# Performance work log

Measured on AMD Instinct MI355X. Metric: run time of the kernel, lower is better.

## Reference

```python
import jax, jax.numpy as jnp
import numpy as np

D_MODEL = 1024
N_HEADS = 16
HEAD_DIM = D_MODEL // N_HEADS
WINDOW = 256


def setup_inputs() -> dict:
    key = jax.random.key(0)
    k1, k2, k3 = jax.random.split(key, 3)
    x = jax.random.normal(k1, (1, 4096, D_MODEL), dtype=jnp.float32)
    # torch nn.Linear weights: [out_features, in_features]
    W_qkv = jax.random.normal(k2, (3 * D_MODEL, D_MODEL), dtype=jnp.float32) * (D_MODEL ** -0.5)
    W_proj = jax.random.normal(k3, (D_MODEL, D_MODEL), dtype=jnp.float32) * (D_MODEL ** -0.5)
    return {"x": x, "W_qkv": W_qkv, "W_proj": W_proj}


def reference(x, W_qkv, W_proj):
    B, T, D = x.shape
    H, Hd = N_HEADS, HEAD_DIM
    qkv = (x @ W_qkv.T).reshape(B, T, 3, H, Hd)
    qkv = jnp.transpose(qkv, (2, 0, 3, 1, 4))  # [3, B, H, T, Hd]
    q, k, v = qkv[0], qkv[1], qkv[2]
    # causal + sliding-window mask: allowed iff 0 <= i - j < WINDOW
    i = jnp.arange(T)[:, None]
    j = jnp.arange(T)[None, :]
    mask = (j <= i) & (j >= i - (WINDOW - 1))  # [T, T] bool
    scale = Hd ** -0.5
    attn = jnp.einsum('bhid,bhjd->bhij', q, k) * scale
    attn = jnp.where(mask, attn, -jnp.inf)
    attn = jax.nn.softmax(attn, axis=-1)
    out = jnp.einsum('bhij,bhjd->bhid', attn, v)  # [B, H, T, Hd]
    out = jnp.transpose(out, (0, 2, 1, 3)).reshape(B, T, D)
    return out @ W_proj.T
```

## Files before the change

### kernel.cpp

```cpp
#include <hip/hip_runtime.h>
#include <hip/hip_bf16.h>


#define T_SEQ   4096
#define DM      1024
#define NH      16
#define HD      64
#define WIN     256

typedef unsigned short u16_t;
typedef u16_t  u16v8 __attribute__((ext_vector_type(8)));
typedef __bf16 bf16v8 __attribute__((ext_vector_type(8)));
typedef float  f32v4 __attribute__((ext_vector_type(4)));

__device__ __forceinline__ f32v4 mfma_bf16(u16v8 a, u16v8 b, f32v4 c) {
    return __builtin_amdgcn_mfma_f32_16x16x32_bf16(
        __builtin_bit_cast(bf16v8, a), __builtin_bit_cast(bf16v8, b), c, 0, 0, 0);
}

__device__ __forceinline__ u16_t f2bf(float f) {
    unsigned u = __builtin_bit_cast(unsigned, f);
    u += 0x7fffu + ((u >> 16) & 1u);
    return (u16_t)(u >> 16);
}

__device__ __forceinline__ float exp2_fast(float x) {
    return __builtin_amdgcn_exp2f(x);
}

__device__ __forceinline__ void gload_lds16(const u16_t* g, u16_t* l) {
    __builtin_amdgcn_global_load_lds(
        (const __attribute__((address_space(1))) unsigned int*)g,
        (__attribute__((address_space(3))) unsigned int*)l, 16, 0, 0);
}

__global__ void cvt_kernel(const float* __restrict__ in, u16_t* __restrict__ out, int n8) {
    int i = blockIdx.x * blockDim.x + threadIdx.x;
    if (i >= n8) return;
    const float4* p = (const float4*)(in + (size_t)i * 8);
    float4 a = p[0], b = p[1];
    u16v8 o;
    o[0] = f2bf(a.x); o[1] = f2bf(a.y); o[2] = f2bf(a.z); o[3] = f2bf(a.w);
    o[4] = f2bf(b.x); o[5] = f2bf(b.y); o[6] = f2bf(b.z); o[7] = f2bf(b.w);
    *(u16v8*)(out + (size_t)i * 8) = o;
}

template <int BM, int BN, int WN, int WAVES, typename OutT>
__global__ __launch_bounds__(WAVES * 64, 2)
void gemm8p(const u16_t* __restrict__ A, const u16_t* __restrict__ B,
            OutT* __restrict__ C, int M, int N, int K) {
    constexpr int WM  = WAVES / WN;
    constexpr int PWM = BM / WM;
    constexpr int PWN = BN / WN;
    constexpr int M_F = PWM / 16, N_F = PWN / 16;
    constexpr int A_H = M_F / 2, N_H = N_F / 2;
    constexpr int THREADS = WAVES * 64;
    constexpr int RPP = THREADS / 8;

    __shared__ u16_t lA[2][BM * 64];
    __shared__ u16_t lB[2][BN * 64];

    const int tid = threadIdx.x;
    const int l = tid & 63, w = tid >> 6;
    const int lr = l & 15, g = l >> 4;
    const int wrh = w / WN, wcq = w % WN;
    const int arow0 = blockIdx.y * BM, bcol0 = blockIdx.x * BN;
    const int r_st = tid >> 3, c8l = tid & 7;
    const int NT = K >> 6;

    f32v4 acc[M_F][N_F];
#pragma unroll
    for (int m = 0; m < M_F; ++m)
#pragma unroll
        for (int n = 0; n < N_F; ++n) acc[m][n] = f32v4{0.f, 0.f, 0.f, 0.f};

#define GSTAGE(buf, kt0)                                                                \
    do {                                                                                \
        _Pragma("unroll")                                                               \
        for (int p = 0; p < BM / RPP; ++p) {                                            \
            int rr = r_st + p * RPP;                                                    \
            int cs = (c8l ^ (rr & 7)) * 8;                                              \
            gload_lds16(A + (size_t)(arow0 + rr) * K + (kt0) + cs,                      \
                        lA[buf] + (size_t)(rr * 64 + c8l * 8));                         \
        }                                                                               \
        _Pragma("unroll")                                                               \
        for (int p = 0; p < BN / RPP; ++p) {                                            \
            int rr = r_st + p * RPP;                                                    \
            int cs = (c8l ^ (rr & 7)) * 8;                                              \
            gload_lds16(B + (size_t)(bcol0 + rr) * K + (kt0) + cs,                      \
                        lB[buf] + (size_t)(rr * 64 + c8l * 8));                         \
        }                                                                               \
    } while (0)

#define SBAR  do { __builtin_amdgcn_s_barrier(); __builtin_amdgcn_sched_barrier(0); } while (0)

    GSTAGE(0, 0);
    __syncthreads();

    u16v8 af[A_H][2], bfr[N_F][2];

    for (int t = 0; t < NT; ++t) {
        const int cur = t & 1;
        const u16_t* cA = lA[cur];
        const u16_t* cB = lB[cur];
        const bool pre = (t + 1 < NT);

        if (pre) GSTAGE(cur ^ 1, (t + 1) << 6);
#pragma unroll
        for (int mf = 0; mf < A_H; ++mf) {
            int row = wrh * PWM + mf * 16 + lr;
#pragma unroll
            for (int ks = 0; ks < 2; ++ks)
                af[mf][ks] = *(const u16v8*)(cA + row * 64 + (((ks * 4 + g) ^ (row & 7)) * 8));
        }
#pragma unroll
        for (int nf = 0; nf < N_H; ++nf) {
            int row = wcq * PWN + nf * 16 + lr;
#pragma unroll
            for (int ks = 0; ks < 2; ++ks)
                bfr[nf][ks] = *(const u16v8*)(cB + row * 64 + (((ks * 4 + g) ^ (row & 7)) * 8));
        }
        SBAR;
        __builtin_amdgcn_s_setprio(1);
#pragma unroll
        for (int mf = 0; mf < A_H; ++mf)
#pragma unroll
            for (int nf = 0; nf < N_H; ++nf)
#pragma unroll
                for (int ks = 0; ks < 2; ++ks)
                    acc[mf][nf] = mfma_bf16(af[mf][ks], bfr[nf][ks], acc[mf][nf]);
        __builtin_amdgcn_s_setprio(0);
        __builtin_amdgcn_sched_barrier(0);
        SBAR;

#pragma unroll
        for (int nf = N_H; nf < N_F; ++nf) {
            int row = wcq * PWN + nf * 16 + lr;
#pragma unroll
            for (int ks = 0; ks < 2; ++ks)
                bfr[nf][ks] = *(const u16v8*)(cB + row * 64 + (((ks * 4 + g) ^ (row & 7)) * 8));
        }
        SBAR;
        __builtin_amdgcn_s_setprio(1);
#pragma unroll
        for (int mf = 0; mf < A_H; ++mf)
#pragma unroll
            for (int nf = N_H; nf < N_F; ++nf)
#pragma unroll
                for (int ks = 0; ks < 2; ++ks)
                    acc[mf][nf] = mfma_bf16(af[mf][ks], bfr[nf][ks], acc[mf][nf]);
        __builtin_amdgcn_s_setprio(0);
        __builtin_amdgcn_sched_barrier(0);
        SBAR;

#pragma unroll
        for (int mf = 0; mf < A_H; ++mf) {
            int row = wrh * PWM + (A_H + mf) * 16 + lr;
#pragma unroll
            for (int ks = 0; ks < 2; ++ks)
                af[mf][ks] = *(const u16v8*)(cA + row * 64 + (((ks * 4 + g) ^ (row & 7)) * 8));
        }
        SBAR;
        __builtin_amdgcn_s_setprio(1);
#pragma unroll
        for (int mf = 0; mf < A_H; ++mf)
#pragma unroll
            for (int nf = N_H; nf < N_F; ++nf)
#pragma unroll
                for (int ks = 0; ks < 2; ++ks)
                    acc[A_H + mf][nf] = mfma_bf16(af[mf][ks], bfr[nf][ks], acc[A_H + mf][nf]);
        __builtin_amdgcn_s_setprio(0);
        __builtin_amdgcn_sched_barrier(0);
        SBAR;

        __builtin_amdgcn_s_setprio(1);
#pragma unroll
        for (int mf = 0; mf < A_H; ++mf)
#pragma unroll
            for (int nf = 0; nf < N_H; ++nf)
#pragma unroll
                for (int ks = 0; ks < 2; ++ks)
                    acc[A_H + mf][nf] = mfma_bf16(af[mf][ks], bfr[nf][ks], acc[A_H + mf][nf]);
        __builtin_amdgcn_s_setprio(0);
        __builtin_amdgcn_sched_barrier(0);
        if (pre) { asm volatile("s_waitcnt vmcnt(0)" ::: "memory"); }
        __syncthreads();
    }
#undef GSTAGE
#undef SBAR

#pragma unroll
    for (int mf = 0; mf < M_F; ++mf) {
        int crow0 = arow0 + wrh * PWM + mf * 16 + g * 4;
#pragma unroll
        for (int nf = 0; nf < N_F; ++nf) {
            int ccol = bcol0 + wcq * PWN + nf * 16 + lr;
#pragma unroll
            for (int j = 0; j < 4; ++j) {
                float v = acc[mf][nf][j];
                if constexpr (sizeof(OutT) == 2)
                    C[(size_t)(crow0 + j) * N + ccol] = (OutT)f2bf(v);
                else
                    C[(size_t)(crow0 + j) * N + ccol] = (OutT)v;
            }
        }
    }
}

__global__ __launch_bounds__(256) void vtrans_kernel(const u16_t* __restrict__ qkv,
                                                     u16_t* __restrict__ vt) {
    __shared__ u16_t tile[64][72];
    const int t0 = blockIdx.x * 64, h = blockIdx.y;
    const int tid = threadIdx.x;
    {
        int r = tid >> 2, c = (tid & 3) * 16;
        const u16_t* src = qkv + (size_t)(t0 + r) * (3 * DM) + 2 * DM + h * HD + c;
        *(u16v8*)&tile[r][c]     = *(const u16v8*)src;
        *(u16v8*)&tile[r][c + 8] = *(const u16v8*)(src + 8);
    }
    __syncthreads();
    {
        int d = tid >> 2, ts = (tid & 3) * 16;
        u16_t* dst = vt + ((size_t)h * HD + d) * T_SEQ + t0 + ts;
        u16v8 o0, o1;
#pragma unroll
        for (int i = 0; i < 8; ++i) { o0[i] = tile[ts + i][d]; o1[i] = tile[ts + 8 + i][d]; }
        *(u16v8*)dst       = o0;
        *(u16v8*)(dst + 8) = o1;
    }
}

__global__ __launch_bounds__(256) void attn_kernel(const u16_t* __restrict__ qkv,
                                                   const u16_t* __restrict__ vt,
                                                   u16_t* __restrict__ out) {
    __shared__ u16_t lK[2][64 * 64];
    __shared__ u16_t lV[2][64 * 64];
    __shared__ u16_t pbuf[4][16 * 64];

    const int h = blockIdx.y;
    const int q0 = blockIdx.x * 64;
    const int tid = threadIdx.x;
    const int w = tid >> 6, l = tid & 63;
    const int lr = l & 15, g = l >> 4;
    const int i0 = q0 + w * 16;
    u16_t* P = pbuf[w];

    const int r_st = tid >> 3;
    const int c8l  = tid & 7;
    const u16_t* kBase = qkv + DM + h * HD;
    const u16_t* vBase = vt + (size_t)h * HD * T_SEQ;

    u16v8 qf0, qf1;
    {
        const u16_t* qrow = qkv + h * HD + (size_t)(i0 + lr) * (3 * DM) + g * 8;
        qf0 = *(const u16v8*)qrow;
        qf1 = *(const u16v8*)(qrow + 32);
    }
    f32v4 o[4];
#pragma unroll
    for (int n = 0; n < 4; ++n) o[n] = f32v4{0.f, 0.f, 0.f, 0.f};
    float m_run[4], l_run[4];
#pragma unroll
    for (int j = 0; j < 4; ++j) { m_run[j] = -1e30f; l_run[j] = 0.f; }

    const int c0 = (q0 >= WIN) ? q0 - WIN : 0;
    const int nch = ((q0 - c0) >> 6) + 1;

#define STAGE_KV(buf, cc)                                                              \
    do {                                                                               \
        _Pragma("unroll")                                                              \
        for (int p = 0; p < 2; ++p) {                                                  \
            int rr = r_st + p * 32;                                                    \
            int cs = c8l ^ (rr & 7);                                                   \
            gload_lds16(kBase + (size_t)(cc + rr) * (3 * DM) + cs * 8,                 \
                        lK[buf] + (size_t)(rr * 64 + c8l * 8));                        \
            gload_lds16(vBase + (size_t)rr * T_SEQ + (cc) + cs * 8,                    \
                        lV[buf] + (size_t)(rr * 64 + c8l * 8));                        \
        }                                                                              \
    } while (0)

    STAGE_KV(0, c0);

    const float sc = 0.125f * 1.4426950408889634f;

    for (int ci = 0; ci < nch; ++ci) {
        const int c = c0 + (ci << 6);
        const int cur = ci & 1;
        __syncthreads();
        if (ci + 1 < nch) STAGE_KV(cur ^ 1, c + 64);

        const u16_t* K = lK[cur];
        const u16_t* V = lV[cur];

        f32v4 s[4];
#pragma unroll
        for (int kt = 0; kt < 4; ++kt) {
            int krow = kt * 16 + lr;
            u16v8 k0 = *(const u16v8*)(K + krow * 64 + ((g     ^ (krow & 7)) * 8));
            u16v8 k1 = *(const u16v8*)(K + krow * 64 + (((4+g) ^ (krow & 7)) * 8));
            f32v4 z = f32v4{0.f, 0.f, 0.f, 0.f};
            z = mfma_bf16(qf0, k0, z);
            z = mfma_bf16(qf1, k1, z);
            s[kt] = z;
        }

        const bool full = (c + 63 <= i0) && (c >= i0 - 240);
        if (full) {
#pragma unroll
            for (int kt = 0; kt < 4; ++kt)
#pragma unroll
                for (int j = 0; j < 4; ++j) s[kt][j] *= sc;
        } else {
#pragma unroll
            for (int j = 0; j < 4; ++j) {
                const int i = i0 + g * 4 + j;
#pragma unroll
                for (int kt = 0; kt < 4; ++kt) {
                    const int jg = c + kt * 16 + lr;
                    float v = s[kt][j] * sc;
                    const bool okm = (jg <= i) && (jg >= i - (WIN - 1));
                    s[kt][j] = okm ? v : -3e38f;
                }
            }
        }

        float mloc[4], corr[4], rsum[4];
#pragma unroll
        for (int j = 0; j < 4; ++j)
            mloc[j] = fmaxf(fmaxf(s[0][j], s[1][j]), fmaxf(s[2][j], s[3][j]));
#pragma unroll
        for (int d = 1; d < 16; d <<= 1)
#pragma unroll
            for (int j = 0; j < 4; ++j) mloc[j] = fmaxf(mloc[j], __shfl_xor(mloc[j], d, 64));
#pragma unroll
        for (int j = 0; j < 4; ++j) {
            float mnew = fmaxf(m_run[j], mloc[j]);
            corr[j] = exp2_fast(m_run[j] - mnew);
            m_run[j] = mnew;
            rsum[j] = 0.f;
        }
#pragma unroll
        for (int kt = 0; kt < 4; ++kt)
#pragma unroll
            for (int j = 0; j < 4; ++j) {
                float p = exp2_fast(s[kt][j] - m_run[j]);
                rsum[j] += p;
                int rP = g * 4 + j;
                int col = kt * 16 + lr;
                int c8 = col >> 3;
                P[rP * 64 + ((c8 ^ (rP & 7)) * 8 + (col & 7))] = f2bf(p);
            }
#pragma unroll
        for (int d = 1; d < 16; d <<= 1)
#pragma unroll
            for (int j = 0; j < 4; ++j) rsum[j] += __shfl_xor(rsum[j], d, 64);
#pragma unroll
        for (int j = 0; j < 4; ++j) l_run[j] = l_run[j] * corr[j] + rsum[j];
#pragma unroll
        for (int n = 0; n < 4; ++n)
#pragma unroll
            for (int j = 0; j < 4; ++j) o[n][j] *= corr[j];

        u16v8 pa0 = *(const u16v8*)(P + lr * 64 + ((g     ^ (lr & 7)) * 8));
        u16v8 pa1 = *(const u16v8*)(P + lr * 64 + (((4+g) ^ (lr & 7)) * 8));
#pragma unroll
        for (int n = 0; n < 4; ++n) {
            int vrow = n * 16 + lr;
            u16v8 v0 = *(const u16v8*)(V + vrow * 64 + ((g     ^ (vrow & 7)) * 8));
            u16v8 v1 = *(const u16v8*)(V + vrow * 64 + (((4+g) ^ (vrow & 7)) * 8));
            o[n] = mfma_bf16(pa0, v0, o[n]);
            o[n] = mfma_bf16(pa1, v1, o[n]);
        }
    }
#undef STAGE_KV

#pragma unroll
    for (int n = 0; n < 4; ++n)
#pragma unroll
        for (int j = 0; j < 4; ++j) {
            int t = i0 + g * 4 + j;
            out[(size_t)t * DM + h * HD + n * 16 + lr] = f2bf(o[n][j] / l_run[j]);
        }
}

extern "C" void kernel_launch(void* const* d_in, const int* in_sizes, int n_in,
                              void* d_out, int out_size, void* d_ws, size_t ws_size,
                              hipStream_t stream) {
    const float* x     = (const float*)d_in[0];
    const float* wqkv  = (const float*)d_in[1];
    const float* wproj = (const float*)d_in[2];
    float* out = (float*)d_out;
    char* ws = (char*)d_ws;

    u16_t* xb     = (u16_t*)(ws);
    u16_t* wqkvb  = (u16_t*)(ws + (size_t)(8u << 20));
    u16_t* wprojb = (u16_t*)(ws + (size_t)(14u << 20));
    u16_t* qkvb   = (u16_t*)(ws + (size_t)(16u << 20));
    u16_t* vt     = (u16_t*)(ws + (size_t)(40u << 20));
    u16_t* attnb  = (u16_t*)(ws);

    const int n8x = T_SEQ * DM / 8, n8q = 3 * DM * DM / 8, n8p = DM * DM / 8;
    cvt_kernel<<<(n8x + 255) / 256, 256, 0, stream>>>(x, xb, n8x);
    cvt_kernel<<<(n8q + 255) / 256, 256, 0, stream>>>(wqkv, wqkvb, n8q);
    cvt_kernel<<<(n8p + 255) / 256, 256, 0, stream>>>(wproj, wprojb, n8p);

    gemm8p<256, 256, 4, 8, u16_t><<<dim3(3 * DM / 256, T_SEQ / 256), 512, 0, stream>>>(
        xb, wqkvb, qkvb, T_SEQ, 3 * DM, DM);

    vtrans_kernel<<<dim3(T_SEQ / 64, NH), 256, 0, stream>>>(qkvb, vt);

    attn_kernel<<<dim3(T_SEQ / 64, NH), 256, 0, stream>>>(qkvb, vt, attnb);

    gemm8p<128, 128, 2, 4, float><<<dim3(DM / 128, T_SEQ / 128), 256, 0, stream>>>(
        attnb, wprojb, out, T_SEQ, DM, DM);
}
```

Baseline: 179.6 us.

## Replace double-buffered GEMM with a four-slot K=32 LDS ring and deeper prefetch

Restructures both bf16 GEMMs so the K loop runs in 32-wide stages through a four-slot shared-memory ring. Three stages are kept in flight, gated by counted vmcnt waits, and each stage needs only one barrier. This replaces the previous 64-wide double buffer, which had several barriers per iteration and a full vmcnt(0) drain. Total LDS use stays the same. The aim is to hide global-load latency and cut synchronisation, at the cost of shorter MFMA bursts per barrier and a new swizzle pattern.

```diff
diff --git a/kernel.cpp b/kernel.cpp
--- a/kernel.cpp
+++ b/kernel.cpp
@@ -47,26 +47,26 @@
 
 template <int BM, int BN, int WN, int WAVES, typename OutT>
 __global__ __launch_bounds__(WAVES * 64, 2)
-void gemm8p(const u16_t* __restrict__ A, const u16_t* __restrict__ B,
-            OutT* __restrict__ C, int M, int N, int K) {
+void gemm_ring(const u16_t* __restrict__ A, const u16_t* __restrict__ B,
+               OutT* __restrict__ C, int M, int N, int K) {
     constexpr int WM  = WAVES / WN;
     constexpr int PWM = BM / WM;
     constexpr int PWN = BN / WN;
     constexpr int M_F = PWM / 16, N_F = PWN / 16;
-    constexpr int A_H = M_F / 2, N_H = N_F / 2;
+    constexpr int N_H = N_F / 2;
     constexpr int THREADS = WAVES * 64;
-    constexpr int RPP = THREADS / 8;
-
-    __shared__ u16_t lA[2][BM * 64];
-    __shared__ u16_t lB[2][BN * 64];
+    constexpr int RP = THREADS / 4;
+
+    __shared__ u16_t lA[4 * BM * 32];
+    __shared__ u16_t lB[4 * BN * 32];
 
     const int tid = threadIdx.x;
     const int l = tid & 63, w = tid >> 6;
     const int lr = l & 15, g = l >> 4;
     const int wrh = w / WN, wcq = w % WN;
     const int arow0 = blockIdx.y * BM, bcol0 = blockIdx.x * BN;
-    const int r_st = tid >> 3, c8l = tid & 7;
-    const int NT = K >> 6;
+    const int rq = tid >> 2, cq = tid & 3;
+    const int NS = K >> 5;
 
     f32v4 acc[M_F][N_F];
 #pragma unroll
@@ -74,120 +74,69 @@
 #pragma unroll
         for (int n = 0; n < N_F; ++n) acc[m][n] = f32v4{0.f, 0.f, 0.f, 0.f};
 
-#define GSTAGE(buf, kt0)                                                                \
+#define GSTAGE(s_)                                                                      \
     do {                                                                                \
+        const int k0_ = (s_) << 5, sl_ = (s_) & 3;                                      \
         _Pragma("unroll")                                                               \
-        for (int p = 0; p < BM / RPP; ++p) {                                            \
-            int rr = r_st + p * RPP;                                                    \
-            int cs = (c8l ^ (rr & 7)) * 8;                                              \
-            gload_lds16(A + (size_t)(arow0 + rr) * K + (kt0) + cs,                      \
-                        lA[buf] + (size_t)(rr * 64 + c8l * 8));                         \
+        for (int p = 0; p < BM / RP; ++p) {                                             \
+            int r = rq + p * RP;                                                        \
+            int cs = cq ^ ((r >> 1) & 3);                                               \
+            gload_lds16(A + (size_t)(arow0 + r) * K + k0_ + cs * 8,                     \
+                        lA + sl_ * (BM * 32) + r * 32 + cq * 8);                        \
         }                                                                               \
         _Pragma("unroll")                                                               \
-        for (int p = 0; p < BN / RPP; ++p) {                                            \
-            int rr = r_st + p * RPP;                                                    \
-            int cs = (c8l ^ (rr & 7)) * 8;                                              \
-            gload_lds16(B + (size_t)(bcol0 + rr) * K + (kt0) + cs,                      \
-                        lB[buf] + (size_t)(rr * 64 + c8l * 8));                         \
+        for (int p = 0; p < BN / RP; ++p) {                                             \
+            int r = rq + p * RP;                                                        \
+            int cs = cq ^ ((r >> 1) & 3);                                               \
+            gload_lds16(B + (size_t)(bcol0 + r) * K + k0_ + cs * 8,                     \
+                        lB + sl_ * (BN * 32) + r * 32 + cq * 8);                        \
         }                                                                               \
     } while (0)
 
-#define SBAR  do { __builtin_amdgcn_s_barrier(); __builtin_amdgcn_sched_barrier(0); } while (0)
-
-    GSTAGE(0, 0);
-    __syncthreads();
-
-    u16v8 af[A_H][2], bfr[N_F][2];
-
-    for (int t = 0; t < NT; ++t) {
-        const int cur = t & 1;
-        const u16_t* cA = lA[cur];
-        const u16_t* cB = lB[cur];
-        const bool pre = (t + 1 < NT);
-
-        if (pre) GSTAGE(cur ^ 1, (t + 1) << 6);
-#pragma unroll
-        for (int mf = 0; mf < A_H; ++mf) {
+    GSTAGE(0); GSTAGE(1); GSTAGE(2);
+
+    for (int s = 0; s < NS; ++s) {
+        if (s < NS - 2)       { asm volatile("s_waitcnt vmcnt(8)" ::: "memory"); }
+        else if (s == NS - 2) { asm volatile("s_waitcnt vmcnt(4)" ::: "memory"); }
+        else                  { asm volatile("s_waitcnt vmcnt(0)" ::: "memory"); }
+        __builtin_amdgcn_s_barrier();
+        __builtin_amdgcn_sched_barrier(0);
+        if (s + 3 < NS) GSTAGE(s + 3);
+
+        const u16_t* sA = lA + (s & 3) * (BM * 32);
+        const u16_t* sB = lB + (s & 3) * (BN * 32);
+        u16v8 a[M_F], b[N_F];
+#pragma unroll
+        for (int mf = 0; mf < M_F; ++mf) {
             int row = wrh * PWM + mf * 16 + lr;
-#pragma unroll
-            for (int ks = 0; ks < 2; ++ks)
-                af[mf][ks] = *(const u16v8*)(cA + row * 64 + (((ks * 4 + g) ^ (row & 7)) * 8));
+            a[mf] = *(const u16v8*)(sA + row * 32 + (g ^ ((row >> 1) & 3)) * 8);
         }
 #pragma unroll
         for (int nf = 0; nf < N_H; ++nf) {
             int row = wcq * PWN + nf * 16 + lr;
-#pragma unroll
-            for (int ks = 0; ks < 2; ++ks)
-                bfr[nf][ks] = *(const u16v8*)(cB + row * 64 + (((ks * 4 + g) ^ (row & 7)) * 8));
-        }
-        SBAR;
+            b[nf] = *(const u16v8*)(sB + row * 32 + (g ^ ((row >> 1) & 3)) * 8);
+        }
         __builtin_amdgcn_s_setprio(1);
 #pragma unroll
-        for (int mf = 0; mf < A_H; ++mf)
+        for (int mf = 0; mf < M_F; ++mf)
 #pragma unroll
             for (int nf = 0; nf < N_H; ++nf)
-#pragma unroll
-                for (int ks = 0; ks < 2; ++ks)
-                    acc[mf][nf] = mfma_bf16(af[mf][ks], bfr[nf][ks], acc[mf][nf]);
+                acc[mf][nf] = mfma_bf16(a[mf], b[nf], acc[mf][nf]);
         __builtin_amdgcn_s_setprio(0);
-        __builtin_amdgcn_sched_barrier(0);
-        SBAR;
-
 #pragma unroll
         for (int nf = N_H; nf < N_F; ++nf) {
             int row = wcq * PWN + nf * 16 + lr;
-#pragma unroll
-            for (int ks = 0; ks < 2; ++ks)
-                bfr[nf][ks] = *(const u16v8*)(cB + row * 64 + (((ks * 4 + g) ^ (row & 7)) * 8));
-        }
-        SBAR;
+            b[nf] = *(const u16v8*)(sB + row * 32 + (g ^ ((row >> 1) & 3)) * 8);
+        }
         __builtin_amdgcn_s_setprio(1);
 #pragma unroll
-        for (int mf = 0; mf < A_H; ++mf)
+        for (int mf = 0; mf < M_F; ++mf)
 #pragma unroll
             for (int nf = N_H; nf < N_F; ++nf)
-#pragma unroll
-                for (int ks = 0; ks < 2; ++ks)
-                    acc[mf][nf] = mfma_bf16(af[mf][ks], bfr[nf][ks], acc[mf][nf]);
+                acc[mf][nf] = mfma_bf16(a[mf], b[nf], acc[mf][nf]);
         __builtin_amdgcn_s_setprio(0);
-        __builtin_amdgcn_sched_barrier(0);
-        SBAR;
-
-#pragma unroll
-        for (int mf = 0; mf < A_H; ++mf) {
-            int row = wrh * PWM + (A_H + mf) * 16 + lr;
-#pragma unroll
-            for (int ks = 0; ks < 2; ++ks)
-                af[mf][ks] = *(const u16v8*)(cA + row * 64 + (((ks * 4 + g) ^ (row & 7)) * 8));
-        }
-        SBAR;
-        __builtin_amdgcn_s_setprio(1);
-#pragma unroll
-        for (int mf = 0; mf < A_H; ++mf)
-#pragma unroll
-            for (int nf = N_H; nf < N_F; ++nf)
-#pragma unroll
-                for (int ks = 0; ks < 2; ++ks)
-                    acc[A_H + mf][nf] = mfma_bf16(af[mf][ks], bfr[nf][ks], acc[A_H + mf][nf]);
-        __builtin_amdgcn_s_setprio(0);
-        __builtin_amdgcn_sched_barrier(0);
-        SBAR;
-
-        __builtin_amdgcn_s_setprio(1);
-#pragma unroll
-        for (int mf = 0; mf < A_H; ++mf)
-#pragma unroll
-            for (int nf = 0; nf < N_H; ++nf)
-#pragma unroll
-                for (int ks = 0; ks < 2; ++ks)
-                    acc[A_H + mf][nf] = mfma_bf16(af[mf][ks], bfr[nf][ks], acc[A_H + mf][nf]);
-        __builtin_amdgcn_s_setprio(0);
-        __builtin_amdgcn_sched_barrier(0);
-        if (pre) { asm volatile("s_waitcnt vmcnt(0)" ::: "memory"); }
-        __syncthreads();
     }
 #undef GSTAGE
-#undef SBAR
 
 #pragma unroll
     for (int mf = 0; mf < M_F; ++mf) {
@@ -404,13 +353,13 @@
     cvt_kernel<<<(n8q + 255) / 256, 256, 0, stream>>>(wqkv, wqkvb, n8q);
     cvt_kernel<<<(n8p + 255) / 256, 256, 0, stream>>>(wproj, wprojb, n8p);
 
-    gemm8p<256, 256, 4, 8, u16_t><<<dim3(3 * DM / 256, T_SEQ / 256), 512, 0, stream>>>(
+    gemm_ring<256, 256, 4, 8, u16_t><<<dim3(3 * DM / 256, T_SEQ / 256), 512, 0, stream>>>(
         xb, wqkvb, qkvb, T_SEQ, 3 * DM, DM);
 
     vtrans_kernel<<<dim3(T_SEQ / 64, NH), 256, 0, stream>>>(qkvb, vt);
 
     attn_kernel<<<dim3(T_SEQ / 64, NH), 256, 0, stream>>>(qkvb, vt, attnb);
 
-    gemm8p<128, 128, 2, 4, float><<<dim3(DM / 128, T_SEQ / 128), 256, 0, stream>>>(
+    gemm_ring<128, 128, 2, 4, float><<<dim3(DM / 128, T_SEQ / 128), 256, 0, stream>>>(
         attnb, wprojb, out, T_SEQ, DM, DM);
 }
```

After: 182.0 us. About the same (+1.3%).
